# Kernel tuning notes

Hardware: AMD Instinct MI355X
Metric: run time of the kernel (lower is better)

## Reference

```python
import jax, jax.numpy as jnp
import numpy as np
import math

# ---- module hyperparams (from init_kwargs) ----
L = 10            # number of hash-grid levels
DIM = 4           # features per level
LOG2T = 16
T = 1 << LOG2T    # hash table size per level
BASE = 16         # base resolution
PLS = 2.0         # per_level_scale
SCALE_MULTI = 0.5
HID = 64
IN_DIM = L * DIM  # 40
OUT_DIM = 13      # 1 + 12
N = 1_000_000

# growth factor b = exp((ln(finest) - ln(base)) / (L - 1)), finest = base * pls**L
B_GROWTH = math.exp((math.log(BASE * PLS ** L) - math.log(BASE)) / (L - 1))
RES = [int(math.floor(BASE * B_GROWTH ** l)) for l in range(L)]

PRIMES = np.array([1, 2654435761, 805459861], dtype=np.uint32)
# 8 corner offsets of a voxel
OFFS = np.array([[i, j, k] for i in (0, 1) for j in (0, 1) for k in (0, 1)], dtype=np.uint32)


def _hash_coords(c):
    # c: uint32 [N, 8, 3] -> int32 [N, 8] indices into table of size T
    p = jnp.asarray(PRIMES)
    h = (c[..., 0] * p[0]) ^ (c[..., 1] * p[1]) ^ (c[..., 2] * p[2])
    return (h & jnp.uint32(T - 1)).astype(jnp.int32)


def _encode(x, tables):
    # x: [N,3] in [0,1]; tables: [L, T, DIM] -> [N, DIM, L]
    offs_u = jnp.asarray(OFFS)                      # uint32 [8,3]
    offs_b = jnp.asarray(OFFS.astype(bool))         # bool   [8,3]
    feats = []
    for l in range(L):
        xs = x * RES[l]
        bottom = jnp.floor(xs)
        frac = xs - bottom                          # [N,3]
        corners = bottom.astype(jnp.uint32)[:, None, :] + offs_u[None]  # [N,8,3]
        idx = _hash_coords(corners)                 # [N,8]
        cf = tables[l][idx]                         # [N,8,DIM] gather
        # trilinear weights: prod over dims of frac (if offset==1) else (1-frac)
        w = jnp.prod(jnp.where(offs_b[None], frac[:, None, :], 1.0 - frac[:, None, :]), axis=-1)  # [N,8]
        feats.append(jnp.einsum('nc,ncd->nd', w, cf))  # [N,DIM]
    return jnp.stack(feats, axis=-1)                # [N, DIM, L]


def setup_inputs() -> dict:
    key = jax.random.key(0)
    ks = jax.random.split(key, 10)
    x = jax.random.uniform(ks[0], (N, 3), dtype=jnp.float32)
    cr = jax.random.uniform(ks[1], (N,), dtype=jnp.float32)
    tables = jax.random.uniform(ks[2], (L, T, DIM), dtype=jnp.float32, minval=-1e-4, maxval=1e-4)
    gain = math.sqrt(2.0)  # calculate_gain('relu')

    def xavier(k, fan_in, fan_out):
        a = gain * math.sqrt(6.0 / (fan_in + fan_out))
        return jax.random.uniform(k, (fan_in, fan_out), dtype=jnp.float32, minval=-a, maxval=a)

    W1 = xavier(ks[3], IN_DIM, HID)
    b1 = jnp.zeros((HID,), jnp.float32)
    W2 = xavier(ks[4], HID, HID)
    b2 = jnp.zeros((HID,), jnp.float32)
    W3 = xavier(ks[5], HID, OUT_DIM)
    b3 = jnp.zeros((OUT_DIM,), jnp.float32)
    return {"x": x, "cr": cr, "tables": tables,
            "W1": W1, "b1": b1, "W2": W2, "b2": b2, "W3": W3, "b3": b3}


def reference(x, cr, tables, W1, b1, W2, b2, W3, b3):
    enc = _encode(x, tables)                        # [N, DIM, L]
    cr_s = cr.reshape(-1) * SCALE_MULTI             # [N]
    n = jnp.arange(L, dtype=jnp.float32).reshape(1, 1, L)
    denom = PLS * 4.0 * n * cr_s[:, None, None]     # [N,1,L]
    erf_x = 1.0 / jnp.sqrt(jnp.maximum(denom, 1e-12))  # safe_div/safe_sqrt; erf(huge)=1 at n=0
    scaling = jax.lax.erf(erf_x)
    h = (enc * scaling).reshape(-1, IN_DIM)         # [N, 40]
    h = jax.nn.selu(h @ W1 + b1)
    h = jax.nn.selu(h @ W2 + b2)
    return h @ W3 + b3                              # [N, 13]
```

## Files before the change

kernel.cpp:

```cpp
#include <hip/hip_runtime.h>
#include <cmath>

typedef unsigned int uint32;
typedef __bf16 bf16;
typedef __bf16 bf16x8 __attribute__((ext_vector_type(8)));
typedef float f32x4 __attribute__((ext_vector_type(4)));

#define LVLS 10
#define TSIZE 65536
#define TMASK 65535u
#define PRIME2 2654435761u
#define PRIME3 805459861u

#define WOFF_W1 0
#define WOFF_W2 4096
#define WOFF_W3 8192
#define W_ELEMS 9216
#define DQ_OFF 18432
#define SC_OFF 18496
#define TAB_OFF_B 18560
#define TAB_ELEMS_F (LVLS * TSIZE * 4)
#define WS_NEEDED ((size_t)TAB_OFF_B + (size_t)TAB_ELEMS_F)

struct KParams { float resf[LVLS]; };

__global__ void scale_kernel(const float* __restrict__ tables, unsigned* __restrict__ scales) {
  int tid = blockIdx.x * 256 + threadIdx.x;
  int i4 = tid * 4;
  if (i4 >= TAB_ELEMS_F) return;
  float4 v = *(const float4*)(tables + i4);
  float m = fmaxf(fmaxf(fabsf(v.x), fabsf(v.y)), fmaxf(fabsf(v.z), fabsf(v.w)));
#pragma unroll
  for (int off = 32; off; off >>= 1) m = fmaxf(m, __shfl_xor(m, off, 64));
  if ((threadIdx.x & 63) == 0) {
    int l = i4 >> 18;
    atomicMax(scales + l, __float_as_uint(m));
  }
}

__global__ void quant_kernel(const float* __restrict__ W1, const float* __restrict__ W2,
                             const float* __restrict__ W3, const float* __restrict__ tables,
                             char* __restrict__ ws8, int do_tab) {
  int tid = blockIdx.x * 256 + threadIdx.x;
  bf16* wsb = (bf16*)ws8;
  if (tid < W_ELEMS) {
    float v;
    if (tid < 4096) {
      int n = tid >> 6, k = tid & 63;
      v = (k < 40) ? W1[k * 64 + n] : 0.f;
    } else if (tid < 8192) {
      int t2 = tid - 4096; int n = t2 >> 6, k = t2 & 63;
      v = W2[k * 64 + n];
    } else {
      int t3 = tid - 8192; int n = t3 >> 6, k = t3 & 63;
      v = (n < 13) ? W3[k * 13 + n] : 0.f;
    }
    wsb[tid] = (bf16)v;
  }
  const unsigned* scales = (const unsigned*)(ws8 + SC_OFF);
  if (tid < LVLS) {
    float s = __uint_as_float(scales[tid]);
    ((float*)(ws8 + DQ_OFF))[tid] = s * (1.0f / 127.0f);
  }
  if (do_tab) {
    int i4 = tid * 4;
    if (i4 < TAB_ELEMS_F) {
      float4 v = *(const float4*)(tables + i4);
      int l = i4 >> 18;
      float s = __uint_as_float(scales[l]);
      float r = (s > 0.f) ? 127.f / s : 0.f;
      int q0 = (int)rintf(fminf(fmaxf(v.x * r, -127.f), 127.f));
      int q1 = (int)rintf(fminf(fmaxf(v.y * r, -127.f), 127.f));
      int q2 = (int)rintf(fminf(fmaxf(v.z * r, -127.f), 127.f));
      int q3 = (int)rintf(fminf(fmaxf(v.w * r, -127.f), 127.f));
      unsigned p = (q0 & 0xff) | ((q1 & 0xff) << 8) | ((q2 & 0xff) << 16) | ((q3 & 0xff) << 24);
      *(unsigned*)(ws8 + TAB_OFF_B + i4) = p;
    }
  }
}

__device__ __forceinline__ float selu_f(float v) {
  float neg = 1.6732632423543772f * (__expf(v) - 1.0f);
  return 1.0507009873554805f * (v > 0.f ? v : neg);
}

__device__ __forceinline__ void gemm_stage(const bf16* __restrict__ Arow,
                                           const bf16* __restrict__ Bbase,
                                           const float* __restrict__ bvec,
                                           bf16* __restrict__ Hwr, int lr) {
  float bias[4];
#pragma unroll
  for (int nt = 0; nt < 4; ++nt) bias[nt] = bvec[nt * 16 + lr];
  f32x4 acc[4][4];
#pragma unroll
  for (int ms = 0; ms < 4; ++ms)
#pragma unroll
    for (int nt = 0; nt < 4; ++nt) {
      f32x4 a = {bias[nt], bias[nt], bias[nt], bias[nt]};
      acc[ms][nt] = a;
    }
  bf16x8 Bf[2][4];
#pragma unroll
  for (int ks = 0; ks < 2; ++ks)
#pragma unroll
    for (int nt = 0; nt < 4; ++nt)
      Bf[ks][nt] = *(const bf16x8*)(Bbase + nt * 1024 + ks * 32);
#pragma unroll
  for (int ks = 0; ks < 2; ++ks) {
    bf16x8 Af[4];
#pragma unroll
    for (int ms = 0; ms < 4; ++ms) Af[ms] = *(const bf16x8*)(Arow + ms * 1152 + ks * 32);
#pragma unroll
    for (int ms = 0; ms < 4; ++ms)
#pragma unroll
      for (int nt = 0; nt < 4; ++nt)
        acc[ms][nt] = __builtin_amdgcn_mfma_f32_16x16x32_bf16(Af[ms], Bf[ks][nt], acc[ms][nt], 0, 0, 0);
  }
#pragma unroll
  for (int ms = 0; ms < 4; ++ms)
#pragma unroll
    for (int nt = 0; nt < 4; ++nt)
#pragma unroll
      for (int r = 0; r < 4; ++r)
        Hwr[(ms * 16 + r) * 72 + nt * 16 + lr] = (bf16)selu_f(acc[ms][nt][r]);
}

template <bool TB>
__global__ __launch_bounds__(256, 4)
void ngp_fused(const float* __restrict__ x, const float* __restrict__ cr,
               const float* __restrict__ tables, const char* __restrict__ ws8,
               const float* __restrict__ b1, const float* __restrict__ b2,
               const float* __restrict__ b3, float* __restrict__ out,
               int N, KParams kp) {
  __shared__ bf16 Hbuf[256 * 72];
  const int tid = threadIdx.x;
  const int n = blockIdx.x * 256 + tid;
  const int ncl = (n < N) ? n : 0;

  const float px = x[ncl * 3 + 0];
  const float py = x[ncl * 3 + 1];
  const float pz = x[ncl * 3 + 2];
  const float crv = cr[ncl];
  const float* dq = (const float*)(ws8 + DQ_OFF);

  float feat[40];
#pragma unroll
  for (int l = 0; l < LVLS; ++l) {
    const float rs = kp.resf[l];
    float xs = px * rs, ys = py * rs, zs = pz * rs;
    float bx = floorf(xs), by = floorf(ys), bz = floorf(zs);
    float fx = xs - bx, fy = ys - by, fz = zs - bz;
    uint32 cx = (uint32)bx, cy = (uint32)by, cz = (uint32)bz;
    uint32 hx0 = cx, hx1 = cx + 1u;
    uint32 hy0 = cy * PRIME2, hy1 = hy0 + PRIME2;
    uint32 hz0 = cz * PRIME3, hz1 = hz0 + PRIME3;
    uint32 idx[8];
    idx[0] = (hx0 ^ hy0 ^ hz0) & TMASK; idx[1] = (hx0 ^ hy0 ^ hz1) & TMASK;
    idx[2] = (hx0 ^ hy1 ^ hz0) & TMASK; idx[3] = (hx0 ^ hy1 ^ hz1) & TMASK;
    idx[4] = (hx1 ^ hy0 ^ hz0) & TMASK; idx[5] = (hx1 ^ hy0 ^ hz1) & TMASK;
    idx[6] = (hx1 ^ hy1 ^ hz0) & TMASK; idx[7] = (hx1 ^ hy1 ^ hz1) & TMASK;

    float f[8][4];
    if (TB) {
      const unsigned* tb = ((const unsigned*)(ws8 + TAB_OFF_B)) + l * TSIZE;
#pragma unroll
      for (int c = 0; c < 8; ++c) {
        unsigned q = tb[idx[c]];
        f[c][0] = (float)(signed char)(q & 0xff);
        f[c][1] = (float)(signed char)((q >> 8) & 0xff);
        f[c][2] = (float)(signed char)((q >> 16) & 0xff);
        f[c][3] = (float)(signed char)(q >> 24);
      }
    } else {
      const float4* tb = ((const float4*)tables) + l * TSIZE;
#pragma unroll
      for (int c = 0; c < 8; ++c) {
        float4 q = tb[idx[c]];
        f[c][0] = q.x; f[c][1] = q.y; f[c][2] = q.z; f[c][3] = q.w;
      }
    }
    float wx1 = fx, wx0 = 1.f - fx, wy1 = fy, wy0 = 1.f - fy, wz1 = fz, wz0 = 1.f - fz;
    float wxy00 = wx0 * wy0, wxy01 = wx0 * wy1, wxy10 = wx1 * wy0, wxy11 = wx1 * wy1;
    float w[8] = {wxy00 * wz0, wxy00 * wz1, wxy01 * wz0, wxy01 * wz1,
                  wxy10 * wz0, wxy10 * wz1, wxy11 * wz0, wxy11 * wz1};
    float a0 = 0.f, a1 = 0.f, a2 = 0.f, a3 = 0.f;
#pragma unroll
    for (int c = 0; c < 8; ++c) {
      a0 = fmaf(w[c], f[c][0], a0);
      a1 = fmaf(w[c], f[c][1], a1);
      a2 = fmaf(w[c], f[c][2], a2);
      a3 = fmaf(w[c], f[c][3], a3);
    }
    float s = erff(rsqrtf(fmaxf(4.0f * (float)l * crv, 1e-12f)));
    if (TB) s *= dq[l];
    feat[0 * 10 + l] = a0 * s;
    feat[1 * 10 + l] = a1 * s;
    feat[2 * 10 + l] = a2 * s;
    feat[3 * 10 + l] = a3 * s;
  }

  {
    bf16* row = Hbuf + tid * 72;
#pragma unroll
    for (int c = 0; c < 5; ++c) {
      bf16x8 v;
#pragma unroll
      for (int j = 0; j < 8; ++j) v[j] = (bf16)feat[c * 8 + j];
      *(bf16x8*)(row + c * 8) = v;
    }
    bf16x8 z;
#pragma unroll
    for (int j = 0; j < 8; ++j) z[j] = (bf16)0.f;
    *(bf16x8*)(row + 40) = z;
    *(bf16x8*)(row + 48) = z;
    *(bf16x8*)(row + 56) = z;
  }
  __syncthreads();

  const int w = tid >> 6;
  const int lane = tid & 63;
  const int lr = lane & 15;
  const int quad = lane >> 4;
  const bf16* wsb = (const bf16*)ws8;

  const bf16* Arow = Hbuf + (w * 64 + lr) * 72 + quad * 8;
  bf16* Hwr = Hbuf + (w * 64 + quad * 4) * 72;

  gemm_stage(Arow, wsb + WOFF_W1 + lr * 64 + quad * 8, b1, Hwr, lr);
  __syncthreads();
  gemm_stage(Arow, wsb + WOFF_W2 + lr * 64 + quad * 8, b2, Hwr, lr);
  __syncthreads();

  {
    float b3v = (lr < 13) ? b3[lr] : 0.f;
    f32x4 acc3[4];
#pragma unroll
    for (int ms = 0; ms < 4; ++ms) {
      f32x4 a = {b3v, b3v, b3v, b3v};
      acc3[ms] = a;
    }
    const bf16* B3b = wsb + WOFF_W3 + lr * 64 + quad * 8;
    bf16x8 B3[2];
    B3[0] = *(const bf16x8*)(B3b);
    B3[1] = *(const bf16x8*)(B3b + 32);
#pragma unroll
    for (int ks = 0; ks < 2; ++ks) {
      bf16x8 Af[4];
#pragma unroll
      for (int ms = 0; ms < 4; ++ms) Af[ms] = *(const bf16x8*)(Arow + ms * 1152 + ks * 32);
#pragma unroll
      for (int ms = 0; ms < 4; ++ms)
        acc3[ms] = __builtin_amdgcn_mfma_f32_16x16x32_bf16(Af[ms], B3[ks], acc3[ms], 0, 0, 0);
    }
    const int rbase = blockIdx.x * 256 + w * 64 + quad * 4;
#pragma unroll
    for (int ms = 0; ms < 4; ++ms)
#pragma unroll
      for (int r = 0; r < 4; ++r) {
        int rowg = rbase + ms * 16 + r;
        if (lr < 13 && rowg < N) out[rowg * 13 + lr] = acc3[ms][r];
      }
  }
}

extern "C" void kernel_launch(void* const* d_in, const int* in_sizes, int n_in,
                              void* d_out, int out_size, void* d_ws, size_t ws_size,
                              hipStream_t stream) {
  const float* x      = (const float*)d_in[0];
  const float* cr     = (const float*)d_in[1];
  const float* tables = (const float*)d_in[2];
  const float* W1     = (const float*)d_in[3];
  const float* b1     = (const float*)d_in[4];
  const float* W2     = (const float*)d_in[5];
  const float* b2     = (const float*)d_in[6];
  const float* W3     = (const float*)d_in[7];
  const float* b3     = (const float*)d_in[8];
  float* out = (float*)d_out;
  const int N = in_sizes[1];

  KParams kp;
  double B = exp((log(16.0 * pow(2.0, 10.0)) - log(16.0)) / 9.0);
  for (int l = 0; l < LVLS; ++l) kp.resf[l] = (float)floor(16.0 * pow(B, (double)l));

  char* ws8 = (char*)d_ws;
  const bool tb = ws_size >= WS_NEEDED;

  const int qblocks = (TAB_ELEMS_F / 4 + 255) / 256;
  if (tb) {
    hipMemsetAsync(ws8 + SC_OFF, 0, 64, stream);
    scale_kernel<<<qblocks, 256, 0, stream>>>(tables, (unsigned*)(ws8 + SC_OFF));
    quant_kernel<<<qblocks, 256, 0, stream>>>(W1, W2, W3, tables, ws8, 1);
  } else {
    quant_kernel<<<(W_ELEMS + 255) / 256, 256, 0, stream>>>(W1, W2, W3, tables, ws8, 0);
  }

  int blocks = (N + 255) / 256;
  if (tb)
    ngp_fused<true><<<blocks, 256, 0, stream>>>(x, cr, tables, ws8, b1, b2, b3, out, N, kp);
  else
    ngp_fused<false><<<blocks, 256, 0, stream>>>(x, cr, tables, ws8, b1, b2, b3, out, N, kp);
}
```

Measured before the change: 482.9 us.

## Prefetch next level's hash gathers, use unsigned byte decode, fast erf, coalesced output

Software-pipelines the per-level hash-table gathers so the next level's eight loads are issued before the current level is interpolated, hiding gather latency. The int8 tables are stored with a +128 bias so the decode can use the hardware unsigned-byte-to-float conversions, with the bias removed by an fma. erff is replaced by a polynomial approximation using a fast reciprocal. The final outputs are staged through shared memory and written with coalesced float4 stores. This raises register pressure and adds two block barriers, and the erf approximation slightly changes precision.

Result: slower. 669.3 us (+38.6%).

```diff
diff --git a/kernel.cpp b/kernel.cpp
--- a/kernel.cpp
+++ b/kernel.cpp
@@ -69,19 +69,80 @@
       int l = i4 >> 18;
       float s = __uint_as_float(scales[l]);
       float r = (s > 0.f) ? 127.f / s : 0.f;
-      int q0 = (int)rintf(fminf(fmaxf(v.x * r, -127.f), 127.f));
-      int q1 = (int)rintf(fminf(fmaxf(v.y * r, -127.f), 127.f));
-      int q2 = (int)rintf(fminf(fmaxf(v.z * r, -127.f), 127.f));
-      int q3 = (int)rintf(fminf(fmaxf(v.w * r, -127.f), 127.f));
+      int q0 = (int)rintf(fminf(fmaxf(v.x * r, -127.f), 127.f)) + 128;
+      int q1 = (int)rintf(fminf(fmaxf(v.y * r, -127.f), 127.f)) + 128;
+      int q2 = (int)rintf(fminf(fmaxf(v.z * r, -127.f), 127.f)) + 128;
+      int q3 = (int)rintf(fminf(fmaxf(v.w * r, -127.f), 127.f)) + 128;
       unsigned p = (q0 & 0xff) | ((q1 & 0xff) << 8) | ((q2 & 0xff) << 16) | ((q3 & 0xff) << 24);
       *(unsigned*)(ws8 + TAB_OFF_B + i4) = p;
     }
   }
+}
+
+__device__ __forceinline__ float ub0(uint32 q) {
+#if __has_builtin(__builtin_amdgcn_cvt_f32_ubyte0)
+  return __builtin_amdgcn_cvt_f32_ubyte0(q);
+#else
+  return (float)(q & 0xffu);
+#endif
+}
+__device__ __forceinline__ float ub1(uint32 q) {
+#if __has_builtin(__builtin_amdgcn_cvt_f32_ubyte1)
+  return __builtin_amdgcn_cvt_f32_ubyte1(q);
+#else
+  return (float)((q >> 8) & 0xffu);
+#endif
+}
+__device__ __forceinline__ float ub2(uint32 q) {
+#if __has_builtin(__builtin_amdgcn_cvt_f32_ubyte2)
+  return __builtin_amdgcn_cvt_f32_ubyte2(q);
+#else
+  return (float)((q >> 16) & 0xffu);
+#endif
+}
+__device__ __forceinline__ float ub3(uint32 q) {
+#if __has_builtin(__builtin_amdgcn_cvt_f32_ubyte3)
+  return __builtin_amdgcn_cvt_f32_ubyte3(q);
+#else
+  return (float)(q >> 24);
+#endif
+}
+
+__device__ __forceinline__ float rcp_fast(float v) {
+#if __has_builtin(__builtin_amdgcn_rcpf)
+  return __builtin_amdgcn_rcpf(v);
+#else
+  return 1.0f / v;
+#endif
+}
+
+__device__ __forceinline__ float erf_fast(float xv) {
+  float t = rcp_fast(fmaf(0.3275911f, xv, 1.0f));
+  float p = fmaf(fmaf(fmaf(fmaf(1.061405429f, t, -1.453152027f),
+                           t, 1.421413741f), t, -0.284496736f), t, 0.254829592f);
+  p *= t;
+  float e = __expf(-xv * xv);
+  return fmaf(-p, e, 1.0f);
 }
 
 __device__ __forceinline__ float selu_f(float v) {
   float neg = 1.6732632423543772f * (__expf(v) - 1.0f);
   return 1.0507009873554805f * (v > 0.f ? v : neg);
+}
+
+__device__ __forceinline__ void level_idx(float px, float py, float pz, float rs,
+                                          uint32* idx, float& fx, float& fy, float& fz) {
+  float xs = px * rs, ys = py * rs, zs = pz * rs;
+  float bx = floorf(xs), by = floorf(ys), bz = floorf(zs);
+  fx = xs - bx; fy = ys - by; fz = zs - bz;
+  uint32 cx = (uint32)bx, cy = (uint32)by, cz = (uint32)bz;
+  uint32 hx0 = cx, hx1 = cx + 1u;
+  uint32 hy0 = cy * PRIME2, hy1 = hy0 + PRIME2;
+  uint32 hz0 = cz * PRIME3, hz1 = hz0 + PRIME3;
+  idx[0] = (hx0 ^ hy0 ^ hz0) & TMASK; idx[1] = (hx0 ^ hy0 ^ hz1) & TMASK;
+  idx[2] = (hx0 ^ hy1 ^ hz0) & TMASK; idx[3] = (hx0 ^ hy1 ^ hz1) & TMASK;
+  idx[4] = (hx1 ^ hy0 ^ hz0) & TMASK; idx[5] = (hx1 ^ hy0 ^ hz1) & TMASK;
+  idx[6] = (hx1 ^ hy1 ^ hz0) & TMASK; idx[7] = (hx1 ^ hy1 ^ hz1) & TMASK;
 }
 
 __device__ __forceinline__ void gemm_stage(const bf16* __restrict__ Arow,
@@ -132,7 +193,7 @@
                const float* __restrict__ b1, const float* __restrict__ b2,
                const float* __restrict__ b3, float* __restrict__ out,
                int N, KParams kp) {
-  __shared__ bf16 Hbuf[256 * 72];
+  __shared__ __align__(16) bf16 Hbuf[256 * 72];
   const int tid = threadIdx.x;
   const int n = blockIdx.x * 256 + tid;
   const int ncl = (n < N) ? n : 0;
@@ -144,59 +205,82 @@
   const float* dq = (const float*)(ws8 + DQ_OFF);
 
   float feat[40];
-#pragma unroll
-  for (int l = 0; l < LVLS; ++l) {
-    const float rs = kp.resf[l];
-    float xs = px * rs, ys = py * rs, zs = pz * rs;
-    float bx = floorf(xs), by = floorf(ys), bz = floorf(zs);
-    float fx = xs - bx, fy = ys - by, fz = zs - bz;
-    uint32 cx = (uint32)bx, cy = (uint32)by, cz = (uint32)bz;
-    uint32 hx0 = cx, hx1 = cx + 1u;
-    uint32 hy0 = cy * PRIME2, hy1 = hy0 + PRIME2;
-    uint32 hz0 = cz * PRIME3, hz1 = hz0 + PRIME3;
-    uint32 idx[8];
-    idx[0] = (hx0 ^ hy0 ^ hz0) & TMASK; idx[1] = (hx0 ^ hy0 ^ hz1) & TMASK;
-    idx[2] = (hx0 ^ hy1 ^ hz0) & TMASK; idx[3] = (hx0 ^ hy1 ^ hz1) & TMASK;
-    idx[4] = (hx1 ^ hy0 ^ hz0) & TMASK; idx[5] = (hx1 ^ hy0 ^ hz1) & TMASK;
-    idx[6] = (hx1 ^ hy1 ^ hz0) & TMASK; idx[7] = (hx1 ^ hy1 ^ hz1) & TMASK;
-
-    float f[8][4];
-    if (TB) {
-      const unsigned* tb = ((const unsigned*)(ws8 + TAB_OFF_B)) + l * TSIZE;
+  if (TB) {
+    const uint32* tb8 = (const uint32*)(ws8 + TAB_OFF_B);
+    uint32 qA[8];
+    float fxA, fyA, fzA;
+    {
+      uint32 idxA[8];
+      level_idx(px, py, pz, kp.resf[0], idxA, fxA, fyA, fzA);
+#pragma unroll
+      for (int c = 0; c < 8; ++c) qA[c] = tb8[idxA[c]];
+    }
+#pragma unroll
+    for (int l = 0; l < LVLS; ++l) {
+      uint32 qB[8];
+      float fxB, fyB, fzB;
+      if (l < LVLS - 1) {
+        uint32 idxB[8];
+        level_idx(px, py, pz, kp.resf[l + 1], idxB, fxB, fyB, fzB);
+        const uint32* base = tb8 + (l + 1) * TSIZE;
+#pragma unroll
+        for (int c = 0; c < 8; ++c) qB[c] = base[idxB[c]];
+      }
+      float wx1 = fxA, wx0 = 1.f - fxA, wy1 = fyA, wy0 = 1.f - fyA, wz1 = fzA, wz0 = 1.f - fzA;
+      float wxy00 = wx0 * wy0, wxy01 = wx0 * wy1, wxy10 = wx1 * wy0, wxy11 = wx1 * wy1;
+      float w[8] = {wxy00 * wz0, wxy00 * wz1, wxy01 * wz0, wxy01 * wz1,
+                    wxy10 * wz0, wxy10 * wz1, wxy11 * wz0, wxy11 * wz1};
+      float a0 = 0.f, a1 = 0.f, a2 = 0.f, a3 = 0.f;
 #pragma unroll
       for (int c = 0; c < 8; ++c) {
-        unsigned q = tb[idx[c]];
-        f[c][0] = (float)(signed char)(q & 0xff);
-        f[c][1] = (float)(signed char)((q >> 8) & 0xff);
-        f[c][2] = (float)(signed char)((q >> 16) & 0xff);
-        f[c][3] = (float)(signed char)(q >> 24);
-      }
-    } else {
+        a0 = fmaf(w[c], ub0(qA[c]), a0);
+        a1 = fmaf(w[c], ub1(qA[c]), a1);
+        a2 = fmaf(w[c], ub2(qA[c]), a2);
+        a3 = fmaf(w[c], ub3(qA[c]), a3);
+      }
+      float s = erf_fast(rsqrtf(fmaxf(4.0f * (float)l * crv, 1e-12f))) * dq[l];
+      float off = -128.f * s;
+      feat[0 * 10 + l] = fmaf(a0, s, off);
+      feat[1 * 10 + l] = fmaf(a1, s, off);
+      feat[2 * 10 + l] = fmaf(a2, s, off);
+      feat[3 * 10 + l] = fmaf(a3, s, off);
+      if (l < LVLS - 1) {
+#pragma unroll
+        for (int c = 0; c < 8; ++c) qA[c] = qB[c];
+        fxA = fxB; fyA = fyB; fzA = fzB;
+      }
+    }
+  } else {
+#pragma unroll
+    for (int l = 0; l < LVLS; ++l) {
+      uint32 idx[8];
+      float fx, fy, fz;
+      level_idx(px, py, pz, kp.resf[l], idx, fx, fy, fz);
       const float4* tb = ((const float4*)tables) + l * TSIZE;
+      float f[8][4];
 #pragma unroll
       for (int c = 0; c < 8; ++c) {
         float4 q = tb[idx[c]];
         f[c][0] = q.x; f[c][1] = q.y; f[c][2] = q.z; f[c][3] = q.w;
       }
-    }
-    float wx1 = fx, wx0 = 1.f - fx, wy1 = fy, wy0 = 1.f - fy, wz1 = fz, wz0 = 1.f - fz;
-    float wxy00 = wx0 * wy0, wxy01 = wx0 * wy1, wxy10 = wx1 * wy0, wxy11 = wx1 * wy1;
-    float w[8] = {wxy00 * wz0, wxy00 * wz1, wxy01 * wz0, wxy01 * wz1,
-                  wxy10 * wz0, wxy10 * wz1, wxy11 * wz0, wxy11 * wz1};
-    float a0 = 0.f, a1 = 0.f, a2 = 0.f, a3 = 0.f;
-#pragma unroll
-    for (int c = 0; c < 8; ++c) {
-      a0 = fmaf(w[c], f[c][0], a0);
-      a1 = fmaf(w[c], f[c][1], a1);
-      a2 = fmaf(w[c], f[c][2], a2);
-      a3 = fmaf(w[c], f[c][3], a3);
-    }
-    float s = erff(rsqrtf(fmaxf(4.0f * (float)l * crv, 1e-12f)));
-    if (TB) s *= dq[l];
-    feat[0 * 10 + l] = a0 * s;
-    feat[1 * 10 + l] = a1 * s;
-    feat[2 * 10 + l] = a2 * s;
-    feat[3 * 10 + l] = a3 * s;
+      float wx1 = fx, wx0 = 1.f - fx, wy1 = fy, wy0 = 1.f - fy, wz1 = fz, wz0 = 1.f - fz;
+      float wxy00 = wx0 * wy0, wxy01 = wx0 * wy1, wxy10 = wx1 * wy0, wxy11 = wx1 * wy1;
+      float w[8] = {wxy00 * wz0, wxy00 * wz1, wxy01 * wz0, wxy01 * wz1,
+                    wxy10 * wz0, wxy10 * wz1, wxy11 * wz0, wxy11 * wz1};
+      float a0 = 0.f, a1 = 0.f, a2 = 0.f, a3 = 0.f;
+#pragma unroll
+      for (int c = 0; c < 8; ++c) {
+        a0 = fmaf(w[c], f[c][0], a0);
+        a1 = fmaf(w[c], f[c][1], a1);
+        a2 = fmaf(w[c], f[c][2], a2);
+        a3 = fmaf(w[c], f[c][3], a3);
+      }
+      float s = erf_fast(rsqrtf(fmaxf(4.0f * (float)l * crv, 1e-12f)));
+      feat[0 * 10 + l] = a0 * s;
+      feat[1 * 10 + l] = a1 * s;
+      feat[2 * 10 + l] = a2 * s;
+      feat[3 * 10 + l] = a3 * s;
+    }
   }
 
   {
@@ -231,9 +315,9 @@
   gemm_stage(Arow, wsb + WOFF_W2 + lr * 64 + quad * 8, b2, Hwr, lr);
   __syncthreads();
 
+  f32x4 acc3[4];
   {
     float b3v = (lr < 13) ? b3[lr] : 0.f;
-    f32x4 acc3[4];
 #pragma unroll
     for (int ms = 0; ms < 4; ++ms) {
       f32x4 a = {b3v, b3v, b3v, b3v};
@@ -252,14 +336,27 @@
       for (int ms = 0; ms < 4; ++ms)
         acc3[ms] = __builtin_amdgcn_mfma_f32_16x16x32_bf16(Af[ms], B3[ks], acc3[ms], 0, 0, 0);
     }
-    const int rbase = blockIdx.x * 256 + w * 64 + quad * 4;
+  }
+  __syncthreads();
+  float* ob = (float*)Hbuf;
+  if (lr < 13) {
 #pragma unroll
     for (int ms = 0; ms < 4; ++ms)
 #pragma unroll
-      for (int r = 0; r < 4; ++r) {
-        int rowg = rbase + ms * 16 + r;
-        if (lr < 13 && rowg < N) out[rowg * 13 + lr] = acc3[ms][r];
-      }
+      for (int r = 0; r < 4; ++r)
+        ob[(w * 64 + quad * 4 + ms * 16 + r) * 13 + lr] = acc3[ms][r];
+  }
+  __syncthreads();
+  const int base = blockIdx.x * (256 * 13);
+  if ((blockIdx.x + 1) * 256 <= N) {
+    const float4* obv = (const float4*)ob;
+    float4* og = (float4*)(out + base);
+#pragma unroll
+    for (int i = tid; i < 832; i += 256) og[i] = obv[i];
+  } else {
+    const int lim = N * 13 - base;
+    for (int i = tid; i < 256 * 13; i += 256)
+      if (i < lim) out[base + i] = ob[i];
   }
 }
 
```
